# Performance work log

Measured on AMD Instinct MI355X. Metric: run time of the kernel, lower is better.

Reference implementation:

```python
import jax, jax.numpy as jnp
import numpy as np

EMBED = 512  # scale uses embed_size**-0.5 per the original forward (NOT head_size)


def setup_inputs() -> dict:
    key = jax.random.key(0)
    k1, k2, k3, k4 = jax.random.split(key, 4)
    B, T, D, H = 8, 4096, EMBED, 64
    inputs = jax.random.normal(k1, (B, T, D), dtype=jnp.float32)
    Wq = jax.random.normal(k2, (D, H), dtype=jnp.float32) * (D ** -0.5)
    Wk = jax.random.normal(k3, (D, H), dtype=jnp.float32) * (D ** -0.5)
    Wv = jax.random.normal(k4, (D, H), dtype=jnp.float32) * (D ** -0.5)
    return {"inputs": inputs, "Wq": Wq, "Wk": Wk, "Wv": Wv}


def reference(inputs, Wq, Wk, Wv):
    # inputs: [B, T, D]; Wq/Wk/Wv: [D, H]
    B, T, D = inputs.shape
    q = inputs @ Wq  # [B, T, H]
    k = inputs @ Wk  # [B, T, H]
    v = inputs @ Wv  # [B, T, H]
    scale = jnp.asarray(D, inputs.dtype) ** -0.5  # original scales by embed_size**-0.5
    scores = jnp.einsum('bth,bsh->bts', q, k) * scale  # [B, T, T]
    causal = jnp.arange(T)[:, None] >= jnp.arange(T)[None, :]  # lower-triangular
    scores = jnp.where(causal, scores, jnp.asarray(-jnp.inf, scores.dtype))
    weights = jax.nn.softmax(scores, axis=-1)
    # dropout is identity in eval mode
    return weights @ v  # [B, T, H]
```

## Files before the change

kernel.cpp:

```cpp
#include <hip/hip_runtime.h>
#include <hip/hip_bf16.h>
#include <math.h>

#define TSEQ 4096
#define NB 8
#define DEM 512
#define HD 64
#define LP 72
#define QSZ ((size_t)NB * TSEQ * HD)

typedef __attribute__((ext_vector_type(8))) short short8;
typedef __attribute__((ext_vector_type(4))) short short4v;
typedef __attribute__((ext_vector_type(4))) float float4v;

__device__ __forceinline__ short f2bf(float f) {
    union { float f; unsigned u; } v; v.f = f;
    unsigned r = v.u + 0x7fffu + ((v.u >> 16) & 1u);
    return (short)(r >> 16);
}

__device__ __forceinline__ short8 pack8(float4 a, float4 b) {
    union { short8 s; __hip_bfloat162 h[4]; } u;
    u.h[0] = __float22bfloat162_rn(make_float2(a.x, a.y));
    u.h[1] = __float22bfloat162_rn(make_float2(a.z, a.w));
    u.h[2] = __float22bfloat162_rn(make_float2(b.x, b.y));
    u.h[3] = __float22bfloat162_rn(make_float2(b.z, b.w));
    return u.s;
}

__device__ __host__ __forceinline__ int slot_base(int mq) {
    int grp = mq >> 3;
    return 4 * grp * (grp + 1) + (mq & 7) * (grp + 1);
}

__global__ __launch_bounds__(256) void wtr_kernel(
    const float* __restrict__ Wq, const float* __restrict__ Wk,
    const float* __restrict__ Wv, short* __restrict__ wt)
{
    __shared__ float t[64][65];
    const int tid = threadIdx.x;
    const int k0 = blockIdx.x * 64;
    const int m = blockIdx.y;
    const float* W = (m == 0) ? Wq : ((m == 1) ? Wk : Wv);
    const float sc = (m == 0) ? 0.044194173824159216f : 1.0f;

#pragma unroll
    for (int i = 0; i < 4; ++i) {
        int f = tid + 256 * i;
        int k = f >> 4, n4 = (f & 15) * 4;
        float4 wv = *(const float4*)&W[(k0 + k) * HD + n4];
        t[k][n4 + 0] = wv.x; t[k][n4 + 1] = wv.y;
        t[k][n4 + 2] = wv.z; t[k][n4 + 3] = wv.w;
    }
    __syncthreads();
#pragma unroll
    for (int i = 0; i < 4; ++i) {
        int f = tid + 256 * i;
        int n = f >> 4, k4 = (f & 15) * 4;
        short4v o;
        o[0] = f2bf(t[k4 + 0][n] * sc);
        o[1] = f2bf(t[k4 + 1][n] * sc);
        o[2] = f2bf(t[k4 + 2][n] * sc);
        o[3] = f2bf(t[k4 + 3][n] * sc);
        *(short4v*)&wt[(size_t)(m * 64 + n) * DEM + k0 + k4] = o;
    }
}

__global__ __launch_bounds__(512, 4) void qkv_mfma(
    const float* __restrict__ x, const short* __restrict__ wt,
    short* __restrict__ q, short* __restrict__ k, short* __restrict__ vt)
{
    __shared__ float rbuf[6 * 64 * 52];

    const int tid = threadIdx.x;
    const int w = tid >> 6;
    const int lane = tid & 63;
    const int l15 = tid & 15;
    const int quad = (tid >> 4) & 3;
    const int rg = w & 1;
    const int kq = w >> 1;
    const int rbase = blockIdx.x * 32 + rg * 16 + l15;

    const float* xr = x + (size_t)rbase * DEM;
    const short* wp = wt + (size_t)l15 * DEM;

    float4v acc[12] = {};

#pragma unroll
    for (int kc = 0; kc < 4; ++kc) {
        const int k0 = kq * 128 + kc * 32 + quad * 8;
        float4 xa = *(const float4*)&xr[k0];
        float4 xb = *(const float4*)&xr[k0 + 4];
        short8 wf[12];
#pragma unroll
        for (int mt = 0; mt < 12; ++mt)
            wf[mt] = *(const short8*)&wp[(size_t)mt * 16 * DEM + k0];
        short8 xv = pack8(xa, xb);
#pragma unroll
        for (int mt = 0; mt < 12; ++mt)
            acc[mt] = __builtin_amdgcn_mfma_f32_16x16x32_bf16(wf[mt], xv, acc[mt], 0, 0, 0);
    }

    if (kq) {
        float* p = &rbuf[(((kq - 1) * 2 + rg) * 64 + lane) * 52];
#pragma unroll
        for (int mt = 0; mt < 12; ++mt)
            *(float4v*)(p + mt * 4) = acc[mt];
    }
    __syncthreads();
    if (kq) return;

#pragma unroll
    for (int s = 0; s < 3; ++s) {
        const float* p = &rbuf[((s * 2 + rg) * 64 + lane) * 52];
#pragma unroll
        for (int mt = 0; mt < 12; ++mt)
            acc[mt] += *(const float4v*)(p + mt * 4);
    }

#pragma unroll
    for (int mt = 0; mt < 8; ++mt) {
        short* dst = (mt < 4) ? q : k;
        short4v o;
        o[0] = f2bf(acc[mt][0]); o[1] = f2bf(acc[mt][1]);
        o[2] = f2bf(acc[mt][2]); o[3] = f2bf(acc[mt][3]);
        *(short4v*)&dst[(size_t)rbase * HD + (mt & 3) * 16 + quad * 4] = o;
    }
    const int b = rbase >> 12, t = rbase & (TSEQ - 1);
#pragma unroll
    for (int mt = 8; mt < 12; ++mt) {
#pragma unroll
        for (int reg = 0; reg < 4; ++reg) {
            int d = (mt - 8) * 16 + quad * 4 + reg;
            vt[((size_t)(b * HD + d)) * TSEQ + t] = f2bf(acc[mt][reg]);
        }
    }
}

__global__ __launch_bounds__(256, 3) void flash_mfma(
    const short* __restrict__ qw, const short* __restrict__ kw,
    const short* __restrict__ vtw,
    float* __restrict__ pO, float* __restrict__ stS)
{
    __shared__ short kt[64 * LP];
    __shared__ short vt[64 * LP];
    __shared__ short pt[4][32 * LP];

    const int tid = threadIdx.x;
    const int w = tid >> 6;
    const int l15 = tid & 15;
    const int quad = (tid >> 4) & 3;
    const int bx = blockIdx.x;
    const int b = bx & 7;
    const int idx = bx >> 3;

    int mq, j;
    if (idx < 52) {
        int t = idx;
        mq = 31; j = 0;
#pragma unroll 1
        for (int mm = 31; mm >= 7; --mm) {
            int f = (2 * mm + 2) >> 4;
            if (t < f) { mq = mm; j = t; break; }
            t -= f;
        }
    } else {
        int t = idx - 52;
        int kc = t >> 2, p = t & 3;
        mq = 30 - kc - 8 * p;
        j = (2 * mq + 2) >> 4;
    }
    const int s0 = 16 * j;
    const int send = min(16 * (j + 1), 2 * mq + 2);
    const int r0 = mq * 128;
    const int slot = b * 80 + slot_base(mq) + j;

    short8 qf[2][2];
#pragma unroll
    for (int g = 0; g < 2; ++g) {
        const short* qrow = qw + ((size_t)(b * TSEQ + r0 + 32 * w + 16 * g + l15)) * HD;
        qf[g][0] = *(const short8*)(qrow + quad * 8);
        qf[g][1] = *(const short8*)(qrow + 32 + quad * 8);
    }

    float l_lane[2] = {0.f, 0.f};
    float4v O[2][4] = {};

    const int srow = tid >> 3, sc = tid & 7;
    const short* kbase = kw + (size_t)b * TSEQ * HD;
    const short* vbase = vtw + (size_t)b * HD * TSEQ;

    short8 kr0, kr1, vr0, vr1;
    {
        const short* kg = kbase + (size_t)(s0 * 64) * HD;
        const short* vg = vbase + s0 * 64;
        kr0 = *(const short8*)(kg + srow * HD + sc * 8);
        kr1 = *(const short8*)(kg + (srow + 32) * HD + sc * 8);
        vr0 = *(const short8*)(vg + (size_t)srow * TSEQ + sc * 8);
        vr1 = *(const short8*)(vg + (size_t)(srow + 32) * TSEQ + sc * 8);
    }

    for (int st = s0; st < send; ++st) {
        __syncthreads();
        *(short8*)&kt[srow * LP + sc * 8] = kr0;
        *(short8*)&kt[(srow + 32) * LP + sc * 8] = kr1;
        *(short8*)&vt[srow * LP + sc * 8] = vr0;
        *(short8*)&vt[(srow + 32) * LP + sc * 8] = vr1;
        __syncthreads();

        if (st + 1 < send) {
            const short* kg = kbase + (size_t)((st + 1) * 64) * HD;
            const short* vg = vbase + (st + 1) * 64;
            kr0 = *(const short8*)(kg + srow * HD + sc * 8);
            kr1 = *(const short8*)(kg + (srow + 32) * HD + sc * 8);
            vr0 = *(const short8*)(vg + (size_t)srow * TSEQ + sc * 8);
            vr1 = *(const short8*)(vg + (size_t)(srow + 32) * TSEQ + sc * 8);
        }

        float4v S[2][4] = {};
#pragma unroll
        for (int mt = 0; mt < 4; ++mt) {
            short8 a0 = *(const short8*)&kt[(mt * 16 + l15) * LP + quad * 8];
            short8 a1 = *(const short8*)&kt[(mt * 16 + l15) * LP + 32 + quad * 8];
            S[0][mt] = __builtin_amdgcn_mfma_f32_16x16x32_bf16(a0, qf[0][0], S[0][mt], 0, 0, 0);
            S[0][mt] = __builtin_amdgcn_mfma_f32_16x16x32_bf16(a1, qf[0][1], S[0][mt], 0, 0, 0);
            S[1][mt] = __builtin_amdgcn_mfma_f32_16x16x32_bf16(a0, qf[1][0], S[1][mt], 0, 0, 0);
            S[1][mt] = __builtin_amdgcn_mfma_f32_16x16x32_bf16(a1, qf[1][1], S[1][mt], 0, 0, 0);
        }

        if (st >= 2 * mq) {
            const int kb = st * 64;
#pragma unroll
            for (int g = 0; g < 2; ++g) {
                int qg = r0 + 32 * w + 16 * g + l15;
#pragma unroll
                for (int mt = 0; mt < 4; ++mt)
#pragma unroll
                    for (int r = 0; r < 4; ++r)
                        if (kb + mt * 16 + quad * 4 + r > qg) S[g][mt][r] = -INFINITY;
            }
        }

#pragma unroll
        for (int g = 0; g < 2; ++g) {
#pragma unroll
            for (int mt = 0; mt < 4; ++mt) {
                float p0 = __expf(S[g][mt][0]);
                float p1 = __expf(S[g][mt][1]);
                float p2 = __expf(S[g][mt][2]);
                float p3 = __expf(S[g][mt][3]);
                l_lane[g] += (p0 + p1) + (p2 + p3);
                short4v pk;
                pk[0] = f2bf(p0); pk[1] = f2bf(p1);
                pk[2] = f2bf(p2); pk[3] = f2bf(p3);
                *(short4v*)&pt[w][(16 * g + l15) * LP + mt * 16 + quad * 4] = pk;
            }
        }

#pragma unroll
        for (int kf = 0; kf < 2; ++kf) {
            short8 pa0 = *(const short8*)&pt[w][l15 * LP + kf * 32 + quad * 8];
            short8 pa1 = *(const short8*)&pt[w][(16 + l15) * LP + kf * 32 + quad * 8];
#pragma unroll
            for (int nt = 0; nt < 4; ++nt) {
                short8 vb = *(const short8*)&vt[(nt * 16 + l15) * LP + kf * 32 + quad * 8];
                O[0][nt] = __builtin_amdgcn_mfma_f32_16x16x32_bf16(pa0, vb, O[0][nt], 0, 0, 0);
                O[1][nt] = __builtin_amdgcn_mfma_f32_16x16x32_bf16(pa1, vb, O[1][nt], 0, 0, 0);
            }
        }
    }

    float* dest = pO + (size_t)slot * 128 * HD;
#pragma unroll
    for (int g = 0; g < 2; ++g) {
#pragma unroll
        for (int r = 0; r < 4; ++r) {
            size_t row = (size_t)(32 * w + 16 * g + quad * 4 + r) * HD;
#pragma unroll
            for (int nt = 0; nt < 4; ++nt)
                dest[row + nt * 16 + l15] = O[g][nt][r];
        }
        float rs = l_lane[g];
        rs += __shfl_xor(rs, 16, 64);
        rs += __shfl_xor(rs, 32, 64);
        if (quad == 0) stS[slot * 128 + 32 * w + 16 * g + l15] = rs;
    }
}

__global__ __launch_bounds__(256) void merge_kernel(
    float* __restrict__ out, const float* __restrict__ pO,
    const float* __restrict__ stS)
{
    const int tid = threadIdx.x;
    const int row = blockIdx.x * 64 + (tid >> 2);
    const int dq = (tid & 3) * 16;
    const int b = row >> 12, t = row & (TSEQ - 1);
    const int mq = t >> 7, rr = t & 127;
    const int nseg = (2 * mq + 2 + 15) >> 4;
    const int sb = b * 80 + slot_base(mq);

    float denom = 0.f;
    for (int s = 0; s < nseg; ++s) denom += stS[(sb + s) * 128 + rr];
    float inv = 1.0f / denom;

    float4 o[4] = {};
    for (int s = 0; s < nseg; ++s) {
        const float4* pp = (const float4*)
            &pO[((size_t)(sb + s) * 128 + rr) * HD + dq];
#pragma unroll
        for (int i = 0; i < 4; ++i) {
            float4 p = pp[i];
            o[i].x += p.x; o[i].y += p.y;
            o[i].z += p.z; o[i].w += p.w;
        }
    }
    float4* op = (float4*)&out[(size_t)row * HD + dq];
#pragma unroll
    for (int i = 0; i < 4; ++i) {
        o[i].x *= inv; o[i].y *= inv; o[i].z *= inv; o[i].w *= inv;
        op[i] = o[i];
    }
}

extern "C" void kernel_launch(void* const* d_in, const int* in_sizes, int n_in,
                              void* d_out, int out_size, void* d_ws, size_t ws_size,
                              hipStream_t stream) {
    const float* x  = (const float*)d_in[0];
    const float* Wq = (const float*)d_in[1];
    const float* Wk = (const float*)d_in[2];
    const float* Wv = (const float*)d_in[3];
    float* out = (float*)d_out;

    short* q  = (short*)d_ws;
    short* k  = q + QSZ;
    short* vt = k + QSZ;
    short* wt = vt + QSZ;
    float* pO = (float*)(wt + 192 * DEM);
    float* stS = pO + (size_t)640 * 128 * HD;

    wtr_kernel<<<dim3(8, 3), 256, 0, stream>>>(Wq, Wk, Wv, wt);
    qkv_mfma<<<dim3(NB * TSEQ / 32), 512, 0, stream>>>(x, wt, q, k, vt);
    flash_mfma<<<dim3(640), 256, 0, stream>>>(q, k, vt, pO, stS);
    merge_kernel<<<dim3(NB * TSEQ / 64), 256, 0, stream>>>(out, pO, stS);
}
```

Measured before the change: 184.8 us.

## Stage QKV weights in LDS via direct loads and skip merge for single-segment rows

The QKV projection kernel now copies a padded bf16 weight image into LDS in four 128-wide K chunks using global_load_lds, instead of having every wave read weights from global memory and split K across waves with an LDS reduction. Blocks cover 64 rows with 256 threads. The flash kernel normalizes and writes final output directly for query blocks whose causal range fits one segment (mq<=7), so the merge kernel runs only over the remaining rows. Flash occupancy hint is raised to 4 blocks per CU, which may pressure registers.

```diff
diff --git a/kernel.cpp b/kernel.cpp
--- a/kernel.cpp
+++ b/kernel.cpp
@@ -7,6 +7,8 @@
 #define DEM 512
 #define HD 64
 #define LP 72
+#define WIP 136
+#define WIMG 26624
 #define QSZ ((size_t)NB * TSEQ * HD)
 
 typedef __attribute__((ext_vector_type(8))) short short8;
@@ -28,6 +30,13 @@
     return u.s;
 }
 
+__device__ __forceinline__ void gload_lds16(const void* g, void* l) {
+    __builtin_amdgcn_global_load_lds(
+        (const __attribute__((address_space(1))) unsigned int*)g,
+        (__attribute__((address_space(3))) unsigned int*)l,
+        16, 0, 0);
+}
+
 __device__ __host__ __forceinline__ int slot_base(int mq) {
     int grp = mq >> 3;
     return 4 * grp * (grp + 1) + (mq & 7) * (grp + 1);
@@ -35,12 +44,14 @@
 
 __global__ __launch_bounds__(256) void wtr_kernel(
     const float* __restrict__ Wq, const float* __restrict__ Wk,
-    const float* __restrict__ Wv, short* __restrict__ wt)
+    const float* __restrict__ Wv, short* __restrict__ wimg)
 {
     __shared__ float t[64][65];
     const int tid = threadIdx.x;
-    const int k0 = blockIdx.x * 64;
+    const int kb = blockIdx.x;
+    const int k0 = kb * 64;
     const int m = blockIdx.y;
+    const int c = kb >> 1, half = kb & 1;
     const float* W = (m == 0) ? Wq : ((m == 1) ? Wk : Wv);
     const float sc = (m == 0) ? 0.044194173824159216f : 1.0f;
 
@@ -62,60 +73,49 @@
         o[1] = f2bf(t[k4 + 1][n] * sc);
         o[2] = f2bf(t[k4 + 2][n] * sc);
         o[3] = f2bf(t[k4 + 3][n] * sc);
-        *(short4v*)&wt[(size_t)(m * 64 + n) * DEM + k0 + k4] = o;
-    }
-}
-
-__global__ __launch_bounds__(512, 4) void qkv_mfma(
-    const float* __restrict__ x, const short* __restrict__ wt,
+        *(short4v*)&wimg[c * WIMG + (64 * m + n) * WIP + half * 64 + k4] = o;
+    }
+}
+
+__global__ __launch_bounds__(256, 2) void qkv_mfma(
+    const float* __restrict__ x, const short* __restrict__ wimg,
     short* __restrict__ q, short* __restrict__ k, short* __restrict__ vt)
 {
-    __shared__ float rbuf[6 * 64 * 52];
+    __shared__ alignas(16) short wlds[WIMG];
 
     const int tid = threadIdx.x;
     const int w = tid >> 6;
-    const int lane = tid & 63;
     const int l15 = tid & 15;
     const int quad = (tid >> 4) & 3;
-    const int rg = w & 1;
-    const int kq = w >> 1;
-    const int rbase = blockIdx.x * 32 + rg * 16 + l15;
+    const int rbase = blockIdx.x * 64 + w * 16 + l15;
 
     const float* xr = x + (size_t)rbase * DEM;
-    const short* wp = wt + (size_t)l15 * DEM;
-
     float4v acc[12] = {};
 
-#pragma unroll
-    for (int kc = 0; kc < 4; ++kc) {
-        const int k0 = kq * 128 + kc * 32 + quad * 8;
-        float4 xa = *(const float4*)&xr[k0];
-        float4 xb = *(const float4*)&xr[k0 + 4];
-        short8 wf[12];
-#pragma unroll
-        for (int mt = 0; mt < 12; ++mt)
-            wf[mt] = *(const short8*)&wp[(size_t)mt * 16 * DEM + k0];
-        short8 xv = pack8(xa, xb);
-#pragma unroll
-        for (int mt = 0; mt < 12; ++mt)
-            acc[mt] = __builtin_amdgcn_mfma_f32_16x16x32_bf16(wf[mt], xv, acc[mt], 0, 0, 0);
-    }
-
-    if (kq) {
-        float* p = &rbuf[(((kq - 1) * 2 + rg) * 64 + lane) * 52];
-#pragma unroll
-        for (int mt = 0; mt < 12; ++mt)
-            *(float4v*)(p + mt * 4) = acc[mt];
-    }
-    __syncthreads();
-    if (kq) return;
-
-#pragma unroll
-    for (int s = 0; s < 3; ++s) {
-        const float* p = &rbuf[((s * 2 + rg) * 64 + lane) * 52];
-#pragma unroll
-        for (int mt = 0; mt < 12; ++mt)
-            acc[mt] += *(const float4v*)(p + mt * 4);
+    for (int c = 0; c < 4; ++c) {
+        __syncthreads();
+        {
+            const char* gsrc = (const char*)(wimg + c * WIMG) + tid * 16;
+            char* ldst = (char*)wlds + tid * 16;
+#pragma unroll
+            for (int i = 0; i < 13; ++i)
+                gload_lds16(gsrc + i * 4096, ldst + i * 4096);
+        }
+        __syncthreads();
+
+#pragma unroll
+        for (int ks = 0; ks < 4; ++ks) {
+            const int k0 = c * 128 + ks * 32 + quad * 8;
+            float4 xa = *(const float4*)&xr[k0];
+            float4 xb = *(const float4*)&xr[k0 + 4];
+            short8 xv = pack8(xa, xb);
+            const int lk = ks * 32 + quad * 8;
+#pragma unroll
+            for (int mt = 0; mt < 12; ++mt) {
+                short8 wf = *(const short8*)&wlds[(mt * 16 + l15) * WIP + lk];
+                acc[mt] = __builtin_amdgcn_mfma_f32_16x16x32_bf16(wf, xv, acc[mt], 0, 0, 0);
+            }
+        }
     }
 
 #pragma unroll
@@ -137,9 +137,9 @@
     }
 }
 
-__global__ __launch_bounds__(256, 3) void flash_mfma(
+__global__ __launch_bounds__(256, 4) void flash_mfma(
     const short* __restrict__ qw, const short* __restrict__ kw,
-    const short* __restrict__ vtw,
+    const short* __restrict__ vtw, float* __restrict__ out,
     float* __restrict__ pO, float* __restrict__ stS)
 {
     __shared__ short kt[64 * LP];
@@ -229,7 +229,7 @@
         }
 
         if (st >= 2 * mq) {
-            const int kb = st * 64;
+            const int kb2 = st * 64;
 #pragma unroll
             for (int g = 0; g < 2; ++g) {
                 int qg = r0 + 32 * w + 16 * g + l15;
@@ -237,7 +237,7 @@
                 for (int mt = 0; mt < 4; ++mt)
 #pragma unroll
                     for (int r = 0; r < 4; ++r)
-                        if (kb + mt * 16 + quad * 4 + r > qg) S[g][mt][r] = -INFINITY;
+                        if (kb2 + mt * 16 + quad * 4 + r > qg) S[g][mt][r] = -INFINITY;
             }
         }
 
@@ -270,20 +270,41 @@
         }
     }
 
-    float* dest = pO + (size_t)slot * 128 * HD;
+    float lred[2];
 #pragma unroll
     for (int g = 0; g < 2; ++g) {
-#pragma unroll
-        for (int r = 0; r < 4; ++r) {
-            size_t row = (size_t)(32 * w + 16 * g + quad * 4 + r) * HD;
-#pragma unroll
-            for (int nt = 0; nt < 4; ++nt)
-                dest[row + nt * 16 + l15] = O[g][nt][r];
-        }
         float rs = l_lane[g];
         rs += __shfl_xor(rs, 16, 64);
         rs += __shfl_xor(rs, 32, 64);
-        if (quad == 0) stS[slot * 128 + 32 * w + 16 * g + l15] = rs;
+        lred[g] = rs;
+    }
+
+    if (mq <= 7) {
+#pragma unroll
+        for (int g = 0; g < 2; ++g) {
+            float iv = 1.0f / lred[g];
+#pragma unroll
+            for (int r = 0; r < 4; ++r) {
+                float ir = __shfl(iv, quad * 4 + r, 64);
+                size_t row = (size_t)(b * TSEQ + r0 + 32 * w + 16 * g + quad * 4 + r) * HD;
+#pragma unroll
+                for (int nt = 0; nt < 4; ++nt)
+                    out[row + nt * 16 + l15] = O[g][nt][r] * ir;
+            }
+        }
+    } else {
+        float* dest = pO + (size_t)slot * 128 * HD;
+#pragma unroll
+        for (int g = 0; g < 2; ++g) {
+#pragma unroll
+            for (int r = 0; r < 4; ++r) {
+                size_t row = (size_t)(32 * w + 16 * g + quad * 4 + r) * HD;
+#pragma unroll
+                for (int nt = 0; nt < 4; ++nt)
+                    dest[row + nt * 16 + l15] = O[g][nt][r];
+            }
+            if (quad == 0) stS[slot * 128 + 32 * w + 16 * g + l15] = lred[g];
+        }
     }
 }
 
@@ -292,9 +313,10 @@
     const float* __restrict__ stS)
 {
     const int tid = threadIdx.x;
-    const int row = blockIdx.x * 64 + (tid >> 2);
+    const int bx = blockIdx.x;
+    const int b = bx / 48, loc = bx - b * 48;
+    const int t = 1024 + loc * 64 + (tid >> 2);
     const int dq = (tid & 3) * 16;
-    const int b = row >> 12, t = row & (TSEQ - 1);
     const int mq = t >> 7, rr = t & 127;
     const int nseg = (2 * mq + 2 + 15) >> 4;
     const int sb = b * 80 + slot_base(mq);
@@ -314,7 +336,7 @@
             o[i].z += p.z; o[i].w += p.w;
         }
     }
-    float4* op = (float4*)&out[(size_t)row * HD + dq];
+    float4* op = (float4*)&out[((size_t)b * TSEQ + t) * HD + dq];
 #pragma unroll
     for (int i = 0; i < 4; ++i) {
         o[i].x *= inv; o[i].y *= inv; o[i].z *= inv; o[i].w *= inv;
@@ -334,12 +356,12 @@
     short* q  = (short*)d_ws;
     short* k  = q + QSZ;
     short* vt = k + QSZ;
-    short* wt = vt + QSZ;
-    float* pO = (float*)(wt + 192 * DEM);
+    short* wimg = vt + QSZ;
+    float* pO = (float*)(wimg + 4 * WIMG);
     float* stS = pO + (size_t)640 * 128 * HD;
 
-    wtr_kernel<<<dim3(8, 3), 256, 0, stream>>>(Wq, Wk, Wv, wt);
-    qkv_mfma<<<dim3(NB * TSEQ / 32), 512, 0, stream>>>(x, wt, q, k, vt);
-    flash_mfma<<<dim3(640), 256, 0, stream>>>(q, k, vt, pO, stS);
-    merge_kernel<<<dim3(NB * TSEQ / 64), 256, 0, stream>>>(out, pO, stS);
-}
+    wtr_kernel<<<dim3(8, 3), 256, 0, stream>>>(Wq, Wk, Wv, wimg);
+    qkv_mfma<<<dim3(NB * TSEQ / 64), 256, 0, stream>>>(x, wimg, q, k, vt);
+    flash_mfma<<<dim3(640), 256, 0, stream>>>(q, k, vt, out, pO, stS);
+    merge_kernel<<<dim3(384), 256, 0, stream>>>(out, pO, stS);
+}
```

New measurement: 160.3 us. -13.3%, faster.
